# Kernel tuning notes

Hardware: AMD Instinct MI355X
Metric: run time of the kernel (lower is better)

## Reference

```python
import jax, jax.numpy as jnp
import numpy as np

DIM = 1024
HEADS = 16
HEAD_DIM = DIM // HEADS
T_MAX = 128
V = 12
T = 128
B = 4
N = V * T + 1  # 1537, includes cls token


def setup_inputs() -> dict:
    key = jax.random.key(0)
    ks = jax.random.split(key, 9)
    s = 0.02
    return {
        "x": jax.random.normal(ks[0], (B, N, DIM), dtype=jnp.float32),
        "qkv_w": jax.random.normal(ks[1], (3 * DIM, DIM), dtype=jnp.float32) * s,
        "in_proj_w": jax.random.normal(ks[2], (3 * DIM, DIM), dtype=jnp.float32) * s,
        "in_proj_b": jax.random.normal(ks[3], (3 * DIM,), dtype=jnp.float32) * s,
        "out_proj_w": jax.random.normal(ks[4], (DIM, DIM), dtype=jnp.float32) * s,
        "out_proj_b": jax.random.normal(ks[5], (DIM,), dtype=jnp.float32) * s,
        "proj_w": jax.random.normal(ks[6], (DIM, DIM), dtype=jnp.float32) * s,
        "proj_b": jax.random.normal(ks[7], (DIM,), dtype=jnp.float32) * s,
        "ids_restore": jax.random.randint(ks[8], (B, V * T), 0, 1000000, dtype=jnp.int64),
        "V_input": V,
        "T_input": T,
    }


def _rope_tables(dtype):
    # theta_d = 10000^{-2d/head_dim}, positions 0..T_max (position 0 is the cls slot)
    theta = 10000.0 ** (-jnp.arange(0, HEAD_DIM, 2, dtype=dtype) / HEAD_DIM)  # (hd/2,)
    pos = jnp.arange(1 + T_MAX, dtype=dtype)
    ang = pos[:, None] * theta[None, :]  # (1+T_max, hd/2)
    return jnp.cos(ang), jnp.sin(ang)


def _rotate(t, cos_g, sin_g):
    # t: (B, N, D); cos_g/sin_g: (B, N-1, 1, hd/2) gathered per non-cls token
    b, n, d = t.shape
    t4 = t.reshape(b, n, HEADS, HEAD_DIM)
    re, im = t4[..., ::2], t4[..., 1::2]  # even/odd interleave -> (B,N,H,hd/2)
    # cls token uses position 0: cos=1, sin=0 -> identity rotation, halves concatenated
    cls = jnp.concatenate([re[:, :1], im[:, :1]], axis=-1)  # (B,1,H,hd)
    rest = jnp.concatenate(
        [re[:, 1:] * cos_g - im[:, 1:] * sin_g,
         re[:, 1:] * sin_g + im[:, 1:] * cos_g], axis=-1)  # (B,N-1,H,hd)
    return jnp.concatenate([cls, rest], axis=1).reshape(b, n, d)


def reference(x, qkv_w, in_proj_w, in_proj_b, out_proj_w, out_proj_b,
              proj_w, proj_b, ids_restore, V_input, T_input):
    b, n, d = x.shape
    # --- qkv projection (no bias) ---
    qkv = jnp.einsum('bnd,ed->bne', x, qkv_w)  # (B,N,3D)
    q, k, v = jnp.split(qkv, 3, axis=-1)
    # --- temporal RoPE with ids_restore-based gather ---
    cos_t, sin_t = _rope_tables(x.dtype)  # (1+T_max, hd/2)
    ids_shuffle = jnp.argsort(ids_restore, axis=1)[:, : n - 1] % V_input  # (B,N-1)
    cos_g = cos_t[ids_shuffle + 1][:, :, None, :]  # gather from cos[:,1:] slice
    sin_g = sin_t[ids_shuffle + 1][:, :, None, :]
    q = _rotate(q, cos_g, sin_g)
    k = _rotate(k, cos_g, sin_g)
    # --- nn.MultiheadAttention (batch_first, no mask, eval) ---
    wq, wk, wv = in_proj_w[:d], in_proj_w[d:2 * d], in_proj_w[2 * d:]
    bq, bk, bv = in_proj_b[:d], in_proj_b[d:2 * d], in_proj_b[2 * d:]
    qp = (jnp.einsum('bnd,ed->bne', q, wq) + bq).reshape(b, n, HEADS, HEAD_DIM)
    kp = (jnp.einsum('bnd,ed->bne', k, wk) + bk).reshape(b, n, HEADS, HEAD_DIM)
    vp = (jnp.einsum('bnd,ed->bne', v, wv) + bv).reshape(b, n, HEADS, HEAD_DIM)
    scale = 1.0 / jnp.sqrt(jnp.asarray(HEAD_DIM, x.dtype))
    scores = jnp.einsum('bqhe,bkhe->bhqk', qp * scale, kp)  # (B,H,N,N)
    attn = jax.nn.softmax(scores, axis=-1)
    ctx = jnp.einsum('bhqk,bkhe->bqhe', attn, vp).reshape(b, n, d)
    mha_out = jnp.einsum('bnd,ed->bne', ctx, out_proj_w) + out_proj_b
    # --- final projection ---
    out = jnp.einsum('bnd,ed->bne', mha_out, proj_w) + proj_b
    return out


if __name__ == '__main__':
    inp = setup_inputs()
    print(reference(**inp).shape)
```

## Files before the change

### kernel.cpp

```cpp
#include <hip/hip_runtime.h>
#include <math.h>

#define B_ 4
#define NTOK 1537
#define NH 16
#define NROWS 6148
#define RPAD 6272
#define KDIM 1024
#define NKT 49

#define MP_QKVW0 0
#define MP_IPW0  2048
#define MP_PW0   5120
#define MP_OPWT0 6144
#define MP_QKVT0 6400
#define MP_X0    6656
#define MP_TAB0  12928
#define MP_SORT0 12929
#define MP_TOTAL 12953

typedef __attribute__((ext_vector_type(8))) short short8;
typedef __attribute__((ext_vector_type(4))) float f32x4;
typedef __attribute__((ext_vector_type(16))) float f32x16;
typedef __attribute__((ext_vector_type(4))) unsigned short ushort4v;
typedef __attribute__((ext_vector_type(4))) unsigned int uint4v;
typedef __attribute__((ext_vector_type(2))) unsigned int uint2v;

__device__ __forceinline__ float bf2f(unsigned short u){
  unsigned int x = ((unsigned int)u) << 16;
  return __uint_as_float(x);
}
__device__ __forceinline__ unsigned short f2bf(float f){
  unsigned int x = __float_as_uint(f);
  x += 0x7fff + ((x >> 16) & 1);
  return (unsigned short)(x >> 16);
}
__device__ __forceinline__ unsigned int pack_bf16(float lo, float hi){
  return (unsigned int)f2bf(lo) | ((unsigned int)f2bf(hi) << 16);
}
__device__ __forceinline__ unsigned int pack_bf16_fast(float lo, float hi){
  unsigned int ue = __float_as_uint(lo) + 0x8000u;
  unsigned int uo = __float_as_uint(hi) + 0x8000u;
  return __builtin_amdgcn_perm(uo, ue, 0x07060302u);
}
__device__ __forceinline__ float fast_exp2(float x){
  return __builtin_amdgcn_exp2f(x);
}
__device__ __forceinline__ uint2v permswap(unsigned int a, unsigned int b){
  return __builtin_amdgcn_permlane32_swap(a, b, false, false);
}
__device__ __forceinline__ void gload_lds16(const void* g, void* l){
  __builtin_amdgcn_global_load_lds((const __attribute__((address_space(1))) unsigned int*)g,
                                   (__attribute__((address_space(3))) unsigned int*)l, 16, 0, 0);
}
__device__ __forceinline__ f32x4 mfma16(short8 a, short8 b, f32x4 c){
  return __builtin_amdgcn_mfma_f32_16x16x32_bf16(a, b, c, 0, 0, 0);
}
__device__ __forceinline__ f32x16 mfma32(short8 a, short8 b, f32x16 c){
  return __builtin_amdgcn_mfma_f32_32x32x16_bf16(a, b, c, 0, 0, 0);
}
__device__ __forceinline__ void xcd_swz(int nx, int ny, int& bx, int& by){
  int lin = blockIdx.y * nx + blockIdx.x;
  int cpx = (nx * ny) >> 3;
  int swz = (lin & 7) * cpx + (lin >> 3);
  bx = swz % nx;
  by = swz / nx;
}

__device__ __forceinline__ void cvt_range(const float* __restrict__ src,
                                          unsigned short* __restrict__ dst,
                                          int lblk, int t){
  int i = (lblk*256 + t)*4;
  f32x4 v = *(const f32x4*)(src + i);
  ushort4v o;
  #pragma unroll
  for (int j=0;j<4;j++) o[j] = f2bf(v[j]);
  *(ushort4v*)(dst + i) = o;
}

__global__ __launch_bounds__(256) void mega_prep_kernel(
    const float* __restrict__ x, const float* __restrict__ qkvw,
    const float* __restrict__ ipw, const float* __restrict__ pw,
    const float* __restrict__ opw, const int* __restrict__ ids,
    unsigned short* __restrict__ xb, unsigned short* __restrict__ qkvwb,
    unsigned short* __restrict__ ipwb, unsigned short* __restrict__ pwb,
    unsigned short* __restrict__ opwT, unsigned short* __restrict__ qkvwTv,
    float* __restrict__ ctab, float* __restrict__ stab, int* __restrict__ postab)
{
  __shared__ float Tl[64][65];
  __shared__ int vals[1536];
  int blk = blockIdx.x;
  int t = threadIdx.x;
  if (blk < MP_IPW0){
    cvt_range(qkvw, qkvwb, blk - MP_QKVW0, t);
  } else if (blk < MP_PW0){
    cvt_range(ipw, ipwb, blk - MP_IPW0, t);
  } else if (blk < MP_OPWT0){
    cvt_range(pw, pwb, blk - MP_PW0, t);
  } else if (blk < MP_X0){
    const float* src; unsigned short* dst; int r0;
    int local;
    if (blk < MP_QKVT0){ src = opw;  dst = opwT;   r0 = 0;    local = blk - MP_OPWT0; }
    else               { src = qkvw; dst = qkvwTv; r0 = 2048; local = blk - MP_QKVT0; }
    int ct = local & 15, rt = local >> 4;
    int i = t >> 4, j4 = (t & 15) * 4;
    #pragma unroll
    for (int s = 0; s < 4; s++){
      int rl = s*16 + i;
      f32x4 v = *(const f32x4*)(src + (size_t)(r0 + rt*64 + rl)*1024 + ct*64 + j4);
      Tl[rl][j4+0]=v[0]; Tl[rl][j4+1]=v[1]; Tl[rl][j4+2]=v[2]; Tl[rl][j4+3]=v[3];
    }
    __syncthreads();
    #pragma unroll
    for (int s = 0; s < 4; s++){
      int cl = s*16 + i;
      ushort4v o;
      #pragma unroll
      for (int k=0;k<4;k++) o[k] = f2bf(Tl[j4+k][cl]);
      *(ushort4v*)(dst + (size_t)(ct*64 + cl)*1024 + rt*64 + j4) = o;
    }
  } else if (blk < MP_TAB0){
    size_t i = ((size_t)(blk - MP_X0)*256 + t)*4;
    size_t row = i >> 10;
    ushort4v o;
    if (row < NROWS){
      f32x4 v = *(const f32x4*)(x + i);
      #pragma unroll
      for (int j=0;j<4;j++) o[j] = f2bf(v[j]);
    } else o = (ushort4v)0;
    *(ushort4v*)(xb + i) = o;
  } else if (blk < MP_SORT0){
    for (int i = t; i < 13*32; i += 256){
      int p = i >> 5, j = i & 31;
      float th = powf(10000.f, -(float)j * (1.f/32.f));
      float ang = (float)p * th;
      ctab[i] = cosf(ang);
      stab[i] = sinf(ang);
    }
  } else {
    int local = blk - MP_SORT0;
    int b = local / 6, seg = local % 6;
    const int* src = ids + b*1536;
    for (int i=t; i<1536; i+=256) vals[i] = src[i];
    __syncthreads();
    int i = seg*256 + t;
    int v = vals[i];
    int rank = 0;
    for (int j=0;j<1536;j++){
      int u = vals[j];
      rank += (u < v) || (u == v && j < i);
    }
    postab[b*1536 + rank] = (i % 12) + 1;
  }
}

__global__ __launch_bounds__(256) void rope_kernel(unsigned short* __restrict__ qkv,
                                                   const int* __restrict__ postab,
                                                   const float* __restrict__ ct,
                                                   const float* __restrict__ st){
  int idx = blockIdx.x*256 + threadIdx.x;
  if (idx >= B_*NTOK*NH) return;
  int h = idx & 15;
  int bn = idx >> 4;
  int b = bn / NTOK;
  int n = bn - b*NTOK;
  unsigned short* rowp = qkv + (size_t)bn*2048;
  int pos = (n == 0) ? 0 : postab[b*1536 + (n-1)];
  const float* cr = ct + pos*32;
  const float* sr = st + pos*32;
  #pragma unroll
  for (int part=0; part<2; part++){
    unsigned short* p = rowp + part*1024 + h*64;
    uint4v vv[8];
    #pragma unroll
    for (int i=0;i<8;i++) vv[i] = ((const uint4v*)p)[i];
    unsigned short* tp = (unsigned short*)vv;
    unsigned short ov[64];
    if (n == 0){
      #pragma unroll
      for (int j=0;j<32;j++){ ov[j] = tp[2*j]; ov[32+j] = tp[2*j+1]; }
    } else {
      #pragma unroll
      for (int j=0;j<32;j++){
        float re = bf2f(tp[2*j]), im = bf2f(tp[2*j+1]);
        float c = cr[j], s = sr[j];
        ov[j]    = f2bf(re*c - im*s);
        ov[32+j] = f2bf(re*s + im*c);
      }
    }
    #pragma unroll
    for (int i=0;i<8;i++) ((uint4v*)p)[i] = ((const uint4v*)ov)[i];
  }
}

__device__ __forceinline__ void gemm_body(const unsigned short* __restrict__ A, int lda,
    const unsigned short* __restrict__ W,
    const float* __restrict__ bias, float scale,
    unsigned short* __restrict__ outb, float* __restrict__ outf, int ldo, int mvalid,
    int rowBase, int colBase, unsigned short* __restrict__ kfdst)
{
  __shared__ alignas(16) unsigned short At[128][32];
  __shared__ alignas(16) unsigned short Bt[128][32];
  int t = threadIdx.x, w = t >> 6, lane = t & 63;
  int g = lane >> 4, l15 = lane & 15;
  int rb = (w >> 1) * 64, cb = (w & 1) * 64;
  f32x4 acc[4][4];
  #pragma unroll
  for (int m=0;m<4;m++)
    #pragma unroll
    for (int n=0;n<4;n++) acc[m][n] = 0.f;
  int srow = lane >> 2;
  int scol = ((lane & 3) ^ ((lane >> 3) & 3)) * 8;
  int rc   = (g ^ ((l15 >> 1) & 3)) * 8;
  for (int kb = 0; kb < KDIM; kb += 32){
    __syncthreads();
    #pragma unroll
    for (int i=0;i<2;i++){
      int rr = i*64 + w*16 + srow;
      gload_lds16(A + (size_t)(rowBase + rr)*lda + kb + scol, &At[i*64 + w*16][0]);
      gload_lds16(W + (size_t)(colBase + rr)*KDIM + kb + scol, &Bt[i*64 + w*16][0]);
    }
    __syncthreads();
    short8 af[4], bf[4];
    #pragma unroll
    for (int m=0;m<4;m++) af[m] = *(const short8*)&At[rb + m*16 + l15][rc];
    #pragma unroll
    for (int n=0;n<4;n++) bf[n] = *(const short8*)&Bt[cb + n*16 + l15][rc];
    #pragma unroll
    for (int m=0;m<4;m++)
      #pragma unroll
      for (int n=0;n<4;n++)
        acc[m][n] = mfma16(af[m], bf[n], acc[m][n]);
  }
  if (kfdst){
    #pragma unroll
    for (int m=0;m<4;m++)
      #pragma unroll
      for (int n=0;n<4;n++){
        int col = colBase + cb + n*16 + l15;
        float bv = bias[col];
        int h  = col >> 6;
        int c  = (col >> 4) & 3, hhd = (col >> 3) & 1, j = col & 7;
        #pragma unroll
        for (int r=0;r<4;r++){
          int row = rowBase + rb + m*16 + g*4 + r;
          if (row < mvalid){
            int b  = row / NTOK;
            int n_ = row - b*NTOK;
            size_t off = ((size_t)((b*16 + h)*NKT + (n_ >> 5)))*2048
                       + c*512 + hhd*256 + (n_ & 31)*8 + j;
            kfdst[off] = f2bf(acc[m][n][r] + bv);
          }
        }
      }
    return;
  }
  #pragma unroll
  for (int m=0;m<4;m++)
    #pragma unroll
    for (int n=0;n<4;n++){
      int col = colBase + cb + n*16 + l15;
      float bv = bias ? bias[col] : 0.f;
      #pragma unroll
      for (int r=0;r<4;r++){
        int row = rowBase + rb + m*16 + g*4 + r;
        if (row < mvalid){
          float v = (acc[m][n][r] + bv) * scale;
          if (outf) outf[(size_t)row*ldo + col] = v;
          else      outb[(size_t)row*ldo + col] = f2bf(v);
        }
      }
    }
}

__global__ __launch_bounds__(256) void gemm_kernel(const unsigned short* __restrict__ A, int lda,
    const unsigned short* __restrict__ W,
    const float* __restrict__ bias, float scale,
    unsigned short* __restrict__ outb, float* __restrict__ outf, int ldo, int mvalid)
{
  int bx, by; xcd_swz(RPAD/128, 8, bx, by);
  gemm_body(A, lda, W, bias, scale, outb, outf, ldo, mvalid, bx*128, by*128, nullptr);
}

__global__ __launch_bounds__(256) void gemm_qkv_kernel(const unsigned short* __restrict__ xb,
    const unsigned short* __restrict__ qkvwb, const unsigned short* __restrict__ Wvb,
    const float* __restrict__ ipb, unsigned short* __restrict__ qkb,
    unsigned short* __restrict__ vpb)
{
  int bx, by; xcd_swz(RPAD/128, 24, bx, by);
  bool isV = by >= 16;
  const unsigned short* W = isV ? Wvb : qkvwb;
  const float* bias = isV ? ipb + 2048 : nullptr;
  unsigned short* outb = isV ? vpb : qkb;
  int ldo = isV ? 1024 : 2048;
  int colBase = (isV ? by - 16 : by) * 128;
  gemm_body(xb, 1024, W, bias, 1.f, outb, nullptr, ldo, NROWS, bx*128, colBase, nullptr);
}

__global__ __launch_bounds__(256) void gemm_inproj_kernel(const unsigned short* __restrict__ qkb,
    const unsigned short* __restrict__ ipwb, const float* __restrict__ ipb,
    unsigned short* __restrict__ qpb, unsigned short* __restrict__ kfb)
{
  int z = blockIdx.z;
  int bx, by; xcd_swz(RPAD/128, 8, bx, by);
  const unsigned short* A = qkb + z*1024;
  const unsigned short* W = ipwb + (size_t)z*1024*1024;
  const float* bias = ipb + z*1024;
  if (z == 0)
    gemm_body(A, 2048, W, bias, 0.125f*1.44269504f, qpb, nullptr, 1024, NROWS,
              bx*128, by*128, nullptr);
  else
    gemm_body(A, 2048, W, bias, 1.f, nullptr, nullptr, 0, NROWS,
              bx*128, by*128, kfb);
}

__global__ __launch_bounds__(256) void gemm_prep_kernel(const unsigned short* __restrict__ pwb,
    const unsigned short* __restrict__ opwT, const unsigned short* __restrict__ wv,
    const unsigned short* __restrict__ qkvwTv,
    unsigned short* __restrict__ Wfb, unsigned short* __restrict__ Wvb,
    const float* __restrict__ pw_f, const float* __restrict__ opb,
    const float* __restrict__ pb, float* __restrict__ bfb)
{
  int z = blockIdx.z;
  if (z == 2){
    int lane = threadIdx.x & 63, sub = threadIdx.x >> 6;
    int cbase = (blockIdx.y*8 + blockIdx.x)*16 + sub*4;
    #pragma unroll
    for (int q = 0; q < 4; q++){
      int c = cbase + q;
      const float* row = pw_f + (size_t)c*1024;
      float s = 0.f;
      #pragma unroll
      for (int e=0; e<16; e++) s += row[lane + e*64] * opb[lane + e*64];
      #pragma unroll
      for (int off=1; off<64; off<<=1) s += __shfl_xor(s, off);
      if (lane == 0) bfb[c] = s + pb[c];
    }
    return;
  }
  const unsigned short* A = z ? wv : pwb;
  const unsigned short* W = z ? qkvwTv : opwT;
  unsigned short* outb = z ? Wvb : Wfb;
  gemm_body(A, 1024, W, nullptr, 1.f, outb, nullptr, 1024, 1024,
            blockIdx.x*128, blockIdx.y*128, nullptr);
}

__global__ __launch_bounds__(256) void vfrag_kernel(const unsigned short* __restrict__ vp,
                                                    unsigned short* __restrict__ vf){
  __shared__ alignas(16) unsigned short Tl[32][72];
  int bh = blockIdx.x, kt = blockIdx.y;
  int b = bh >> 4, h = bh & 15;
  int t = threadIdx.x;
  {
    int r = t >> 3, ch = t & 7;
    int key = kt*32 + r;
    uint4v v;
    if (key < NTOK){
      v = *(const uint4v*)(vp + (size_t)(b*NTOK + key)*KDIM + h*64 + ch*8);
    } else v = (uint4v)0;
    *(uint4v*)&Tl[r][ch*8] = v;
  }
  __syncthreads();
  {
    int lane = t & 63, w = t >> 6;
    int l31 = lane & 31, hh = lane >> 5;
    int dblk = w >> 1, c = w & 1;
    unsigned short ov[8];
    #pragma unroll
    for (int j=0;j<8;j++) ov[j] = Tl[c*16 + hh*8 + j][dblk*32 + l31];
    *(uint4v*)(vf + (size_t)(bh*NKT + kt)*2048 + w*512 + lane*8) = *(const uint4v*)ov;
  }
}

__global__ __launch_bounds__(128) void attn_kernel(const unsigned short* __restrict__ qp,
    const unsigned short* __restrict__ kf, const unsigned short* __restrict__ vf,
    unsigned short* __restrict__ ctx)
{
  int bh = blockIdx.x;
  int qt = blockIdx.y*2 + (threadIdx.x >> 6);
  int b = bh >> 4, hd = bh & 15;
  int lane = threadIdx.x & 63;
  int l31 = lane & 31, hh = lane >> 5;
  int qrow = qt*32 + l31;
  int qcl = qrow > NTOK-1 ? NTOK-1 : qrow;
  const unsigned short* qb = qp + (((size_t)(b*NTOK + qcl)*NH + hd) << 6) + hh*8;
  short8 qf[4];
  #pragma unroll
  for (int c=0;c<4;c++) qf[c] = *(const short8*)(qb + c*16);
  const unsigned short* kfb = kf + (size_t)(bh*NKT)*2048 + lane*8;
  const unsigned short* vfb = vf + (size_t)(bh*NKT)*2048 + lane*8;
  float m_ = -3e38f, l_ = 0.f;
  f32x16 o0 = 0.f, o1 = 0.f;

  auto soft_pv = [&](f32x16 cc, short8 va00, short8 va01, short8 va10, short8 va11){
    float t0 = fmaxf(fmaxf(cc[0],cc[1]), fmaxf(cc[2],cc[3]));
    float t1 = fmaxf(fmaxf(cc[4],cc[5]), fmaxf(cc[6],cc[7]));
    float t2 = fmaxf(fmaxf(cc[8],cc[9]), fmaxf(cc[10],cc[11]));
    float t3 = fmaxf(fmaxf(cc[12],cc[13]), fmaxf(cc[14],cc[15]));
    float mx = fmaxf(fmaxf(t0,t1), fmaxf(t2,t3));
    {
      uint2v pr = permswap(__float_as_uint(mx), __float_as_uint(mx));
      mx = fmaxf(__uint_as_float(pr[0]), __uint_as_float(pr[1]));
    }
    if (!__all(mx <= m_ + 11.5f)){
      float mn = fmaxf(m_, mx);
      float al = fast_exp2(m_ - mn);
      m_ = mn;
      l_ *= al;
      #pragma unroll
      for (int i=0;i<16;i++){ o0[i] *= al; o1[i] *= al; }
    }
    float p[16], rs = 0.f;
    #pragma unroll
    for (int i=0;i<16;i++){ p[i] = fast_exp2(cc[i] - m_); }
    #pragma unroll
    for (int i=0;i<16;i++) rs += p[i];
    l_ += rs;
    unsigned int W[8];
    #pragma unroll
    for (int wd=0; wd<8; wd++) W[wd] = pack_bf16_fast(p[2*wd], p[2*wd+1]);
    uint2v e0 = permswap(W[0], W[2]);
    uint2v e1 = permswap(W[1], W[3]);
    uint2v e2 = permswap(W[4], W[6]);
    uint2v e3 = permswap(W[5], W[7]);
    uint4v u0, u1;
    u0[0]=e0[0]; u0[1]=e1[0]; u0[2]=e0[1]; u0[3]=e1[1];
    u1[0]=e2[0]; u1[1]=e3[0]; u1[2]=e2[1]; u1[3]=e3[1];
    short8 pb0, pb1;
    __builtin_memcpy(&pb0, &u0, 16);
    __builtin_memcpy(&pb1, &u1, 16);
    o0 = mfma32(va00, pb0, o0);
    o0 = mfma32(va01, pb1, o0);
    o1 = mfma32(va10, pb0, o1);
    o1 = mfma32(va11, pb1, o1);
  };

  short8 ka[4];
  #pragma unroll
  for (int c=0;c<4;c++) ka[c] = *(const short8*)(kfb + c*512);
  f32x16 cc = 0.f;
  cc = mfma32(ka[0], qf[0], cc);
  cc = mfma32(ka[1], qf[1], cc);
  cc = mfma32(ka[2], qf[2], cc);
  cc = mfma32(ka[3], qf[3], cc);
  #pragma unroll
  for (int c=0;c<4;c++) ka[c] = *(const short8*)(kfb + 2048 + c*512);

  for (int kt=0; kt<48; ++kt){
    const unsigned short* vB = vfb + (size_t)kt*2048;
    short8 va00 = *(const short8*)(vB);
    short8 va01 = *(const short8*)(vB + 512);
    short8 va10 = *(const short8*)(vB + 1024);
    short8 va11 = *(const short8*)(vB + 1536);
    f32x16 cn = 0.f;
    cn = mfma32(ka[0], qf[0], cn);
    cn = mfma32(ka[1], qf[1], cn);
    cn = mfma32(ka[2], qf[2], cn);
    cn = mfma32(ka[3], qf[3], cn);
    int ktn = kt+2 < NKT-1 ? kt+2 : NKT-1;
    const unsigned short* kB = kfb + (size_t)ktn*2048;
    #pragma unroll
    for (int c=0;c<4;c++) ka[c] = *(const short8*)(kB + c*512);
    soft_pv(cc, va00, va01, va10, va11);
    cc = cn;
  }
  {
    const unsigned short* vB = vfb + (size_t)48*2048;
    short8 va00 = *(const short8*)(vB);
    short8 va01 = *(const short8*)(vB + 512);
    short8 va10 = *(const short8*)(vB + 1024);
    short8 va11 = *(const short8*)(vB + 1536);
    #pragma unroll
    for (int i=0;i<16;i++) cc[i] = (i == 0 && hh == 0) ? cc[i] : -1e30f;
    soft_pv(cc, va00, va01, va10, va11);
  }
  {
    uint2v pr = permswap(__float_as_uint(l_), __float_as_uint(l_));
    l_ = __uint_as_float(pr[0]) + __uint_as_float(pr[1]);
  }
  if (qrow < NTOK){
    float inv = 1.f / l_;
    unsigned short* cb = ctx + (((size_t)(b*NTOK + qrow)*NH + hd) << 6) + 4*hh;
    #pragma unroll
    for (int s=0;s<4;s++){
      uint2v u;
      u[0] = pack_bf16(o0[4*s]*inv,   o0[4*s+1]*inv);
      u[1] = pack_bf16(o0[4*s+2]*inv, o0[4*s+3]*inv);
      *(uint2v*)(cb + 8*s) = u;
    }
    #pragma unroll
    for (int s=0;s<4;s++){
      uint2v u;
      u[0] = pack_bf16(o1[4*s]*inv,   o1[4*s+1]*inv);
      u[1] = pack_bf16(o1[4*s+2]*inv, o1[4*s+3]*inv);
      *(uint2v*)(cb + 32 + 8*s) = u;
    }
  }
}

extern "C" void kernel_launch(void* const* d_in, const int* in_sizes, int n_in,
                              void* d_out, int out_size, void* d_ws, size_t ws_size,
                              hipStream_t stream)
{
  const float* x    = (const float*)d_in[0];
  const float* qkvw = (const float*)d_in[1];
  const float* ipw  = (const float*)d_in[2];
  const float* ipb  = (const float*)d_in[3];
  const float* opw  = (const float*)d_in[4];
  const float* opb  = (const float*)d_in[5];
  const float* pw   = (const float*)d_in[6];
  const float* pb   = (const float*)d_in[7];
  const int*   ids  = (const int*)d_in[8];
  float* out = (float*)d_out;

  char* p = (char*)d_ws;
  auto alloc = [&](size_t bytes)->char* {
    char* r = p; p += (bytes + 255) & ~(size_t)255; return r;
  };
  unsigned short* xb     = (unsigned short*)alloc((size_t)RPAD*1024*2);
  unsigned short* qkvwb  = (unsigned short*)alloc((size_t)2048*1024*2);
  unsigned short* ipwb   = (unsigned short*)alloc((size_t)3072*1024*2);
  unsigned short* pwb    = (unsigned short*)alloc((size_t)1024*1024*2);
  unsigned short* opwT   = (unsigned short*)alloc((size_t)1024*1024*2);
  unsigned short* qkvwTv = (unsigned short*)alloc((size_t)1024*1024*2);
  unsigned short* Wfb    = (unsigned short*)alloc((size_t)1024*1024*2);
  unsigned short* Wvb    = (unsigned short*)alloc((size_t)1024*1024*2);
  float*          bfb    = (float*)alloc(1024*4);
  unsigned short* qkb    = (unsigned short*)alloc((size_t)RPAD*2048*2);
  unsigned short* qpb    = (unsigned short*)alloc((size_t)RPAD*1024*2);
  unsigned short* kfb    = (unsigned short*)alloc((size_t)64*NKT*2048*2);
  unsigned short* vpb    = (unsigned short*)alloc((size_t)RPAD*1024*2);
  unsigned short* ctxb   = (unsigned short*)alloc((size_t)RPAD*1024*2);
  int*   postab = (int*)alloc((size_t)B_*1536*4);
  float* ctab   = (float*)alloc(13*32*4);
  float* stab   = (float*)alloc(13*32*4);
  unsigned short* vfb = xb;

  mega_prep_kernel<<<MP_TOTAL, 256, 0, stream>>>(x, qkvw, ipw, pw, opw, ids,
      xb, qkvwb, ipwb, pwb, opwT, qkvwTv, ctab, stab, postab);
  gemm_prep_kernel<<<dim3(8, 8, 3), 256, 0, stream>>>(pwb, opwT, ipwb + (size_t)2048*1024,
                                                      qkvwTv, Wfb, Wvb, pw, opb, pb, bfb);
  gemm_qkv_kernel<<<dim3(RPAD/128, 24), 256, 0, stream>>>(xb, qkvwb, Wvb, ipb, qkb, vpb);
  rope_kernel<<<(B_*NTOK*NH + 255)/256, 256, 0, stream>>>(qkb, postab, ctab, stab);
  gemm_inproj_kernel<<<dim3(RPAD/128, 8, 2), 256, 0, stream>>>(qkb, ipwb, ipb, qpb, kfb);
  vfrag_kernel<<<dim3(B_*NH, NKT), 256, 0, stream>>>(vpb, vfb);
  attn_kernel<<<dim3(B_*NH, 25), 128, 0, stream>>>(qpb, kfb, vfb, ctxb);
  gemm_kernel<<<dim3(RPAD/128, 8), 256, 0, stream>>>(ctxb, 1024, Wfb, bfb, 1.f,
                                                     nullptr, out, 1024, NROWS);
}
```

Measured before the change: 336.1 us.

## Fuse RoPE and V-fragment layout into the QKV GEMM epilogue

The QKV projection GEMM epilogue now applies the rotary embedding directly on the accumulators, pairing even/odd columns with a lane shuffle, and writes the de-interleaved q/k halves. The V columns are written straight into the fragment layout the attention kernel expects. This removes the separate rope and vfrag kernels along with their extra global-memory round trips and launches. In exchange the epilogue does scattered 2-byte stores and extra table loads, and V needs its own buffer instead of reusing xb.

```diff
diff --git a/kernel.cpp b/kernel.cpp
--- a/kernel.cpp
+++ b/kernel.cpp
@@ -154,57 +154,15 @@
   }
 }
 
-__global__ __launch_bounds__(256) void rope_kernel(unsigned short* __restrict__ qkv,
-                                                   const int* __restrict__ postab,
-                                                   const float* __restrict__ ct,
-                                                   const float* __restrict__ st){
-  int idx = blockIdx.x*256 + threadIdx.x;
-  if (idx >= B_*NTOK*NH) return;
-  int h = idx & 15;
-  int bn = idx >> 4;
-  int b = bn / NTOK;
-  int n = bn - b*NTOK;
-  unsigned short* rowp = qkv + (size_t)bn*2048;
-  int pos = (n == 0) ? 0 : postab[b*1536 + (n-1)];
-  const float* cr = ct + pos*32;
-  const float* sr = st + pos*32;
-  #pragma unroll
-  for (int part=0; part<2; part++){
-    unsigned short* p = rowp + part*1024 + h*64;
-    uint4v vv[8];
-    #pragma unroll
-    for (int i=0;i<8;i++) vv[i] = ((const uint4v*)p)[i];
-    unsigned short* tp = (unsigned short*)vv;
-    unsigned short ov[64];
-    if (n == 0){
-      #pragma unroll
-      for (int j=0;j<32;j++){ ov[j] = tp[2*j]; ov[32+j] = tp[2*j+1]; }
-    } else {
-      #pragma unroll
-      for (int j=0;j<32;j++){
-        float re = bf2f(tp[2*j]), im = bf2f(tp[2*j+1]);
-        float c = cr[j], s = sr[j];
-        ov[j]    = f2bf(re*c - im*s);
-        ov[32+j] = f2bf(re*s + im*c);
-      }
-    }
-    #pragma unroll
-    for (int i=0;i<8;i++) ((uint4v*)p)[i] = ((const uint4v*)ov)[i];
-  }
-}
-
-__device__ __forceinline__ void gemm_body(const unsigned short* __restrict__ A, int lda,
-    const unsigned short* __restrict__ W,
-    const float* __restrict__ bias, float scale,
-    unsigned short* __restrict__ outb, float* __restrict__ outf, int ldo, int mvalid,
-    int rowBase, int colBase, unsigned short* __restrict__ kfdst)
+__device__ __forceinline__ void gemm_core(const unsigned short* __restrict__ A, int lda,
+    const unsigned short* __restrict__ W, int rowBase, int colBase,
+    f32x4 (&acc)[4][4])
 {
   __shared__ alignas(16) unsigned short At[128][32];
   __shared__ alignas(16) unsigned short Bt[128][32];
   int t = threadIdx.x, w = t >> 6, lane = t & 63;
   int g = lane >> 4, l15 = lane & 15;
   int rb = (w >> 1) * 64, cb = (w & 1) * 64;
-  f32x4 acc[4][4];
   #pragma unroll
   for (int m=0;m<4;m++)
     #pragma unroll
@@ -232,7 +190,130 @@
       for (int n=0;n<4;n++)
         acc[m][n] = mfma16(af[m], bf[n], acc[m][n]);
   }
-  if (kfdst){
+}
+
+__device__ __forceinline__ void epi_rowmajor(f32x4 (&acc)[4][4],
+    const float* __restrict__ bias, float scale,
+    unsigned short* __restrict__ outb, float* __restrict__ outf, int ldo, int mvalid,
+    int rowBase, int colBase)
+{
+  int t = threadIdx.x, w = t >> 6, lane = t & 63;
+  int g = lane >> 4, l15 = lane & 15;
+  int rb = (w >> 1) * 64, cb = (w & 1) * 64;
+  #pragma unroll
+  for (int m=0;m<4;m++)
+    #pragma unroll
+    for (int n=0;n<4;n++){
+      int col = colBase + cb + n*16 + l15;
+      float bv = bias ? bias[col] : 0.f;
+      #pragma unroll
+      for (int r=0;r<4;r++){
+        int row = rowBase + rb + m*16 + g*4 + r;
+        if (row < mvalid){
+          float v = (acc[m][n][r] + bv) * scale;
+          if (outf) outf[(size_t)row*ldo + col] = v;
+          else      outb[(size_t)row*ldo + col] = f2bf(v);
+        }
+      }
+    }
+}
+
+__global__ __launch_bounds__(256) void gemm_kernel(const unsigned short* __restrict__ A, int lda,
+    const unsigned short* __restrict__ W,
+    const float* __restrict__ bias, float scale,
+    unsigned short* __restrict__ outb, float* __restrict__ outf, int ldo, int mvalid)
+{
+  int bx, by; xcd_swz(RPAD/128, 8, bx, by);
+  f32x4 acc[4][4];
+  gemm_core(A, lda, W, bx*128, by*128, acc);
+  epi_rowmajor(acc, bias, scale, outb, outf, ldo, mvalid, bx*128, by*128);
+}
+
+__global__ __launch_bounds__(256) void gemm_qkv_kernel(const unsigned short* __restrict__ xb,
+    const unsigned short* __restrict__ qkvwb, const unsigned short* __restrict__ Wvb,
+    const float* __restrict__ ipb, const int* __restrict__ postab,
+    const float* __restrict__ ctab, const float* __restrict__ stab,
+    unsigned short* __restrict__ qkb, unsigned short* __restrict__ vf)
+{
+  int bx, by; xcd_swz(RPAD/128, 24, bx, by);
+  bool isV = by >= 16;
+  int rowBase = bx*128;
+  int colBase = (isV ? by - 16 : by) * 128;
+  f32x4 acc[4][4];
+  gemm_core(xb, 1024, isV ? Wvb : qkvwb, rowBase, colBase, acc);
+  int t = threadIdx.x, w = t >> 6, lane = t & 63;
+  int g = lane >> 4, l15 = lane & 15;
+  int rb = (w >> 1) * 64, cb = (w & 1) * 64;
+  if (isV){
+    #pragma unroll
+    for (int m=0;m<4;m++)
+      #pragma unroll
+      for (int n=0;n<4;n++){
+        int col = colBase + cb + n*16 + l15;
+        float bv = ipb[2048 + col];
+        int h = col >> 6, d64 = col & 63;
+        int dblk = d64 >> 5, l31f = d64 & 31;
+        #pragma unroll
+        for (int r=0;r<4;r++){
+          int row = rowBase + rb + m*16 + g*4 + r;
+          if (row < NROWS){
+            int b  = row / NTOK;
+            int n_ = row - b*NTOK;
+            int kt = n_ >> 5, kk = n_ & 31;
+            int c = kk >> 4, hhf = (kk >> 3) & 1, j = kk & 7;
+            size_t off = ((size_t)((b*16 + h)*NKT + kt))*2048
+                       + (dblk*2 + c)*512 + hhf*256 + l31f*8 + j;
+            vf[off] = f2bf(acc[m][n][r] + bv);
+          }
+        }
+      }
+  } else {
+    #pragma unroll
+    for (int m=0;m<4;m++)
+      #pragma unroll
+      for (int r=0;r<4;r++){
+        int row = rowBase + rb + m*16 + g*4 + r;
+        int rowc = row < NROWS ? row : NROWS-1;
+        int b  = rowc / NTOK;
+        int n_ = rowc - b*NTOK;
+        int pos = (n_ == 0) ? 0 : postab[b*1536 + n_ - 1];
+        const float* cr = ctab + pos*32;
+        const float* sr = stab + pos*32;
+        unsigned short* rowp = qkb + (size_t)row*2048;
+        #pragma unroll
+        for (int n=0;n<4;n++){
+          int col = colBase + cb + n*16 + l15;
+          int colh = col & 63;
+          int jj = colh >> 1, odd = colh & 1;
+          float my = acc[m][n][r];
+          float other = __shfl_xor(my, 1);
+          float c_ = cr[jj], s_ = sr[jj];
+          float res = my*c_ + other*(odd ? s_ : -s_);
+          if (row < NROWS)
+            rowp[(col & ~63) | (odd*32 + jj)] = f2bf(res);
+        }
+      }
+  }
+}
+
+__global__ __launch_bounds__(256) void gemm_inproj_kernel(const unsigned short* __restrict__ qkb,
+    const unsigned short* __restrict__ ipwb, const float* __restrict__ ipb,
+    unsigned short* __restrict__ qpb, unsigned short* __restrict__ kfb)
+{
+  int z = blockIdx.z;
+  int bx, by; xcd_swz(RPAD/128, 8, bx, by);
+  int rowBase = bx*128, colBase = by*128;
+  const unsigned short* A = qkb + z*1024;
+  const unsigned short* W = ipwb + (size_t)z*1024*1024;
+  const float* bias = ipb + z*1024;
+  f32x4 acc[4][4];
+  gemm_core(A, 2048, W, rowBase, colBase, acc);
+  if (z == 0){
+    epi_rowmajor(acc, bias, 0.125f*1.44269504f, qpb, nullptr, 1024, NROWS, rowBase, colBase);
+  } else {
+    int t = threadIdx.x, w = t >> 6, lane = t & 63;
+    int g = lane >> 4, l15 = lane & 15;
+    int rb = (w >> 1) * 64, cb = (w & 1) * 64;
     #pragma unroll
     for (int m=0;m<4;m++)
       #pragma unroll
@@ -244,74 +325,16 @@
         #pragma unroll
         for (int r=0;r<4;r++){
           int row = rowBase + rb + m*16 + g*4 + r;
-          if (row < mvalid){
+          if (row < NROWS){
             int b  = row / NTOK;
             int n_ = row - b*NTOK;
             size_t off = ((size_t)((b*16 + h)*NKT + (n_ >> 5)))*2048
                        + c*512 + hhd*256 + (n_ & 31)*8 + j;
-            kfdst[off] = f2bf(acc[m][n][r] + bv);
+            kfb[off] = f2bf(acc[m][n][r] + bv);
           }
         }
       }
-    return;
-  }
-  #pragma unroll
-  for (int m=0;m<4;m++)
-    #pragma unroll
-    for (int n=0;n<4;n++){
-      int col = colBase + cb + n*16 + l15;
-      float bv = bias ? bias[col] : 0.f;
-      #pragma unroll
-      for (int r=0;r<4;r++){
-        int row = rowBase + rb + m*16 + g*4 + r;
-        if (row < mvalid){
-          float v = (acc[m][n][r] + bv) * scale;
-          if (outf) outf[(size_t)row*ldo + col] = v;
-          else      outb[(size_t)row*ldo + col] = f2bf(v);
-        }
-      }
-    }
-}
-
-__global__ __launch_bounds__(256) void gemm_kernel(const unsigned short* __restrict__ A, int lda,
-    const unsigned short* __restrict__ W,
-    const float* __restrict__ bias, float scale,
-    unsigned short* __restrict__ outb, float* __restrict__ outf, int ldo, int mvalid)
-{
-  int bx, by; xcd_swz(RPAD/128, 8, bx, by);
-  gemm_body(A, lda, W, bias, scale, outb, outf, ldo, mvalid, bx*128, by*128, nullptr);
-}
-
-__global__ __launch_bounds__(256) void gemm_qkv_kernel(const unsigned short* __restrict__ xb,
-    const unsigned short* __restrict__ qkvwb, const unsigned short* __restrict__ Wvb,
-    const float* __restrict__ ipb, unsigned short* __restrict__ qkb,
-    unsigned short* __restrict__ vpb)
-{
-  int bx, by; xcd_swz(RPAD/128, 24, bx, by);
-  bool isV = by >= 16;
-  const unsigned short* W = isV ? Wvb : qkvwb;
-  const float* bias = isV ? ipb + 2048 : nullptr;
-  unsigned short* outb = isV ? vpb : qkb;
-  int ldo = isV ? 1024 : 2048;
-  int colBase = (isV ? by - 16 : by) * 128;
-  gemm_body(xb, 1024, W, bias, 1.f, outb, nullptr, ldo, NROWS, bx*128, colBase, nullptr);
-}
-
-__global__ __launch_bounds__(256) void gemm_inproj_kernel(const unsigned short* __restrict__ qkb,
-    const unsigned short* __restrict__ ipwb, const float* __restrict__ ipb,
-    unsigned short* __restrict__ qpb, unsigned short* __restrict__ kfb)
-{
-  int z = blockIdx.z;
-  int bx, by; xcd_swz(RPAD/128, 8, bx, by);
-  const unsigned short* A = qkb + z*1024;
-  const unsigned short* W = ipwb + (size_t)z*1024*1024;
-  const float* bias = ipb + z*1024;
-  if (z == 0)
-    gemm_body(A, 2048, W, bias, 0.125f*1.44269504f, qpb, nullptr, 1024, NROWS,
-              bx*128, by*128, nullptr);
-  else
-    gemm_body(A, 2048, W, bias, 1.f, nullptr, nullptr, 0, NROWS,
-              bx*128, by*128, kfb);
+  }
 }
 
 __global__ __launch_bounds__(256) void gemm_prep_kernel(const unsigned short* __restrict__ pwb,
@@ -341,35 +364,10 @@
   const unsigned short* A = z ? wv : pwb;
   const unsigned short* W = z ? qkvwTv : opwT;
   unsigned short* outb = z ? Wvb : Wfb;
-  gemm_body(A, 1024, W, nullptr, 1.f, outb, nullptr, 1024, 1024,
-            blockIdx.x*128, blockIdx.y*128, nullptr);
-}
-
-__global__ __launch_bounds__(256) void vfrag_kernel(const unsigned short* __restrict__ vp,
-                                                    unsigned short* __restrict__ vf){
-  __shared__ alignas(16) unsigned short Tl[32][72];
-  int bh = blockIdx.x, kt = blockIdx.y;
-  int b = bh >> 4, h = bh & 15;
-  int t = threadIdx.x;
-  {
-    int r = t >> 3, ch = t & 7;
-    int key = kt*32 + r;
-    uint4v v;
-    if (key < NTOK){
-      v = *(const uint4v*)(vp + (size_t)(b*NTOK + key)*KDIM + h*64 + ch*8);
-    } else v = (uint4v)0;
-    *(uint4v*)&Tl[r][ch*8] = v;
-  }
-  __syncthreads();
-  {
-    int lane = t & 63, w = t >> 6;
-    int l31 = lane & 31, hh = lane >> 5;
-    int dblk = w >> 1, c = w & 1;
-    unsigned short ov[8];
-    #pragma unroll
-    for (int j=0;j<8;j++) ov[j] = Tl[c*16 + hh*8 + j][dblk*32 + l31];
-    *(uint4v*)(vf + (size_t)(bh*NKT + kt)*2048 + w*512 + lane*8) = *(const uint4v*)ov;
-  }
+  f32x4 acc[4][4];
+  gemm_core(A, 1024, W, blockIdx.x*128, blockIdx.y*128, acc);
+  epi_rowmajor(acc, nullptr, 1.f, outb, nullptr, 1024, 1024,
+               blockIdx.x*128, blockIdx.y*128);
 }
 
 __global__ __launch_bounds__(128) void attn_kernel(const unsigned short* __restrict__ qp,
@@ -529,21 +527,19 @@
   unsigned short* qkb    = (unsigned short*)alloc((size_t)RPAD*2048*2);
   unsigned short* qpb    = (unsigned short*)alloc((size_t)RPAD*1024*2);
   unsigned short* kfb    = (unsigned short*)alloc((size_t)64*NKT*2048*2);
-  unsigned short* vpb    = (unsigned short*)alloc((size_t)RPAD*1024*2);
+  unsigned short* vfb    = (unsigned short*)alloc((size_t)64*NKT*2048*2);
   unsigned short* ctxb   = (unsigned short*)alloc((size_t)RPAD*1024*2);
   int*   postab = (int*)alloc((size_t)B_*1536*4);
   float* ctab   = (float*)alloc(13*32*4);
   float* stab   = (float*)alloc(13*32*4);
-  unsigned short* vfb = xb;
 
   mega_prep_kernel<<<MP_TOTAL, 256, 0, stream>>>(x, qkvw, ipw, pw, opw, ids,
       xb, qkvwb, ipwb, pwb, opwT, qkvwTv, ctab, stab, postab);
   gemm_prep_kernel<<<dim3(8, 8, 3), 256, 0, stream>>>(pwb, opwT, ipwb + (size_t)2048*1024,
                                                       qkvwTv, Wfb, Wvb, pw, opb, pb, bfb);
-  gemm_qkv_kernel<<<dim3(RPAD/128, 24), 256, 0, stream>>>(xb, qkvwb, Wvb, ipb, qkb, vpb);
-  rope_kernel<<<(B_*NTOK*NH + 255)/256, 256, 0, stream>>>(qkb, postab, ctab, stab);
+  gemm_qkv_kernel<<<dim3(RPAD/128, 24), 256, 0, stream>>>(xb, qkvwb, Wvb, ipb,
+                                                          postab, ctab, stab, qkb, vfb);
   gemm_inproj_kernel<<<dim3(RPAD/128, 8, 2), 256, 0, stream>>>(qkb, ipwb, ipb, qpb, kfb);
-  vfrag_kernel<<<dim3(B_*NH, NKT), 256, 0, stream>>>(vpb, vfb);
   attn_kernel<<<dim3(B_*NH, 25), 128, 0, stream>>>(qpb, kfb, vfb, ctxb);
   gemm_kernel<<<dim3(RPAD/128, 8), 256, 0, stream>>>(ctxb, 1024, Wfb, bfb, 1.f,
                                                      nullptr, out, 1024, NROWS);
```

Result: slower. 386.1 us (+14.9%).
